# Kernel tuning notes

Hardware: AMD Instinct MI355X
Metric: run time of the kernel (lower is better)

Reference implementation:

```python
import jax, jax.numpy as jnp
import numpy as np

N = 30000   # nodes
E = 480000  # edges
IN = 128    # hidden_dim (in_feats)
H = 4       # num_heads
D = 128     # out_feats per head
HD = H * D
NEG_SLOPE = 0.2
BN_EPS = 1e-5


def setup_inputs() -> dict:
    key = jax.random.key(0)
    ks = jax.random.split(key, 12)
    feat = jax.random.normal(ks[0], (N, IN), dtype=jnp.float32)
    src = jax.random.randint(ks[1], (E,), 0, N)
    dst = jax.random.randint(ks[2], (E,), 0, N)
    sc_in = 1.0 / np.sqrt(IN)
    sc_hd = 1.0 / np.sqrt(HD)
    W_fc = jax.random.normal(ks[3], (IN, HD), dtype=jnp.float32) * sc_in
    attn_l = jax.random.normal(ks[4], (H, D), dtype=jnp.float32) * sc_in
    attn_r = jax.random.normal(ks[5], (H, D), dtype=jnp.float32) * sc_in
    W_res = jax.random.normal(ks[6], (IN, HD), dtype=jnp.float32) * sc_in
    bias_gat = jnp.zeros((HD,), dtype=jnp.float32)
    gamma = jnp.ones((HD,), dtype=jnp.float32)
    beta = jnp.zeros((HD,), dtype=jnp.float32)
    W_out = jax.random.normal(ks[7], (HD, IN), dtype=jnp.float32) * sc_hd
    b_out = jnp.zeros((IN,), dtype=jnp.float32)
    return dict(feat=feat, src=src, dst=dst, W_fc=W_fc, attn_l=attn_l,
                attn_r=attn_r, W_res=W_res, bias_gat=bias_gat,
                gamma=gamma, beta=beta, W_out=W_out, b_out=b_out)


def reference(feat, src, dst, W_fc, attn_l, attn_r, W_res, bias_gat,
              gamma, beta, W_out, b_out):
    # --- GATConv (eval mode: dropout off) ---
    h = (feat @ W_fc).reshape(N, H, D)               # projected feats [N,H,D]
    el = jnp.einsum('nhd,hd->nh', h, attn_l)         # [N,H]
    er = jnp.einsum('nhd,hd->nh', h, attn_r)         # [N,H]
    e = el[src] + er[dst]                            # [E,H]
    e = jnp.where(e > 0, e, NEG_SLOPE * e)           # leaky_relu(0.2)
    # segment softmax over edges grouped by destination node
    emax = jax.ops.segment_max(e, dst, num_segments=N)   # [N,H]
    emax = jnp.where(jnp.isfinite(emax), emax, 0.0)      # empty segments
    ex = jnp.exp(e - emax[dst])                          # [E,H]
    denom = jax.ops.segment_sum(ex, dst, num_segments=N) # [N,H]
    a = ex / denom[dst]                                  # [E,H] attention
    msgs = h[src] * a[:, :, None]                        # [E,H,D]
    rst = jax.ops.segment_sum(msgs, dst, num_segments=N) # [N,H,D]
    # residual (in_feats != H*out_feats -> linear res_fc) + bias
    rst = rst + (feat @ W_res).reshape(N, H, D) + bias_gat.reshape(1, H, D)
    # --- fc_out: Flatten -> BatchNorm1d (train stats) -> ReLU -> Linear ---
    x = rst.reshape(N, HD)
    mu = x.mean(axis=0)
    var = x.var(axis=0)
    xn = (x - mu) / jnp.sqrt(var + BN_EPS)
    x = jnp.maximum(gamma * xn + beta, 0.0)
    return x @ W_out + b_out                             # [N, IN]
```

## Files before the change

kernel.cpp:

```cpp
#include <hip/hip_runtime.h>

#define N_  30000
#define E_  480000

typedef short short8 __attribute__((ext_vector_type(8)));
typedef float f32x4  __attribute__((ext_vector_type(4)));
typedef unsigned int u32x4 __attribute__((ext_vector_type(4)));
typedef unsigned int u32x2 __attribute__((ext_vector_type(2)));
union Frag { u32x4 q; short8 v; unsigned short us[8]; };

__device__ __forceinline__ float b2f(unsigned short u){
  union { unsigned int i; float f; } v; v.i = ((unsigned int)u) << 16; return v.f;
}
__device__ __forceinline__ float blo(unsigned int u){
  union { unsigned int i; float f; } v; v.i = u << 16; return v.f;
}
__device__ __forceinline__ float bhi(unsigned int u){
  union { unsigned int i; float f; } v; v.i = u & 0xffff0000u; return v.f;
}
__device__ __forceinline__ unsigned short f2b(float f){
  union { float f; unsigned int u; } v; v.f = f;
  unsigned int u = v.u;
  return (unsigned short)((u + 0x7fffu + ((u >> 16) & 1u)) >> 16);
}

__global__ void k_initconv(const float* __restrict__ Wfc, const float* __restrict__ Wres,
                           const float* __restrict__ Wout, const float* __restrict__ feat,
                           unsigned short* __restrict__ Wt2, unsigned short* __restrict__ WtOut,
                           unsigned short* __restrict__ featb,
                           int* __restrict__ counts, int* __restrict__ cursor){
  int gid = blockIdx.x * 256 + threadIdx.x;
  int stride = gridDim.x * 256;
  if (gid < N_){ counts[gid] = 0; cursor[gid] = 0; }
  const int total1 = 512 * 256;
  const int total2 = 128 * 512;
  for (int i = gid; i < total1 + total2; i += stride){
    if (i < total1){
      int c = i >> 8, k = i & 255;
      float v = (k < 128) ? Wfc[k * 512 + c] : Wres[(k - 128) * 512 + c];
      Wt2[((k >> 7) << 16) + c * 128 + (k & 127)] = f2b(v);
    } else {
      int j = i - total1;
      int n = j >> 9, k = j & 511;
      WtOut[((k >> 7) << 14) + n * 128 + (k & 127)] = f2b(Wout[k * 128 + n]);
    }
  }
  for (int i = gid; i < N_ * 128; i += stride)
    featb[i] = f2b(feat[i]);
}

__global__ __launch_bounds__(128) void k_prep(const float* __restrict__ Wfc,
                                              const float* __restrict__ al,
                                              const float* __restrict__ ar,
                                              float* __restrict__ P){
  int idx = blockIdx.x * 128 + threadIdx.x;
  if (idx >= 1024) return;
  int k = idx >> 3, q = idx & 7;
  int h = q & 3;
  const float* a = (q < 4) ? al : ar;
  const float* wr = Wfc + k * 512 + h * 128;
  const float* av = a + h * 128;
  float s = 0.f;
#pragma unroll 4
  for (int d = 0; d < 128; d++) s += wr[d] * av[d];
  P[k * 8 + q] = s;
}

__global__ __launch_bounds__(256) void k_el(const float* __restrict__ feat,
                                            const float* __restrict__ P,
                                            float* __restrict__ el, float* __restrict__ er){
  __shared__ float sF[32 * 132];
  __shared__ float sP[1024];
  int t = threadIdx.x;
  int n0 = blockIdx.x * 32;
  *reinterpret_cast<f32x4*>(&sP[t * 4]) = *reinterpret_cast<const f32x4*>(P + t * 4);
#pragma unroll
  for (int i = 0; i < 4; i++){
    int c = t + i * 256;
    int r = c >> 5, cw = (c & 31) * 4;
    int gn = n0 + r;
    f32x4 v = {0.f, 0.f, 0.f, 0.f};
    if (gn < N_) v = *reinterpret_cast<const f32x4*>(feat + gn * 128 + cw);
    *reinterpret_cast<f32x4*>(&sF[r * 132 + cw]) = v;
  }
  __syncthreads();
  int node = t >> 3, q = t & 7;
  int gn = n0 + node;
  const float* fr = &sF[node * 132];
  float s = 0.f;
#pragma unroll 2
  for (int k = 0; k < 128; k += 4){
    f32x4 fv = *reinterpret_cast<const f32x4*>(fr + k);
#pragma unroll
    for (int j = 0; j < 4; j++) s += fv[j] * sP[(k + j) * 8 + q];
  }
  if (gn < N_){
    if (q < 4) el[gn * 4 + q] = s;
    else       er[gn * 4 + (q - 4)] = s;
  }
}

__global__ void k_hist(const int* __restrict__ dst, int* __restrict__ counts){
  int e = blockIdx.x * 256 + threadIdx.x;
  if (e < E_) atomicAdd(&counts[dst[e]], 1);
}

__global__ __launch_bounds__(1024) void k_scan(const int* __restrict__ counts,
                                               int* __restrict__ offs){
  __shared__ int wsum[16];
  int t = threadIdx.x;
  int lane = t & 63, w = t >> 6;
  int base = t * 32;
  int vals[32];
  int s = 0;
#pragma unroll
  for (int j = 0; j < 32; j++){
    int idx = base + j;
    int v = (idx < N_) ? counts[idx] : 0;
    vals[j] = s;
    s += v;
  }
  int x = s;
  for (int o = 1; o < 64; o <<= 1){
    int y = __shfl_up(x, o);
    if (lane >= o) x += y;
  }
  if (lane == 63) wsum[w] = x;
  __syncthreads();
  if (t < 16){
    int y = wsum[t];
    for (int o = 1; o < 16; o <<= 1){
      int z = __shfl_up(y, o, 16);
      if (t >= o) y += z;
    }
    wsum[t] = y;
  }
  __syncthreads();
  int wbase = (w > 0) ? wsum[w - 1] : 0;
  int ex = wbase + x - s;
#pragma unroll
  for (int j = 0; j < 32; j++){
    int idx = base + j;
    if (idx <= N_) offs[idx] = ex + vals[j];
  }
}

__global__ void k_edge(const int* __restrict__ src, const int* __restrict__ dst,
                       const float* __restrict__ el, const float* __restrict__ er,
                       float* __restrict__ es_s, int* __restrict__ src_s,
                       const int* __restrict__ offs, int* __restrict__ cursor){
  int e = blockIdx.x * 256 + threadIdx.x;
  if (e >= E_) return;
  int s = src[e], d = dst[e];
  f32x4 a = *reinterpret_cast<const f32x4*>(el + s * 4);
  f32x4 b = *reinterpret_cast<const f32x4*>(er + d * 4);
  f32x4 v = a + b;
#pragma unroll
  for (int i = 0; i < 4; i++) v[i] = v[i] > 0.f ? v[i] : 0.2f * v[i];
  int p = atomicAdd(&cursor[d], 1);
  int pos = offs[d] + p;
  *reinterpret_cast<f32x4*>(es_s + pos * 4) = v;
  src_s[pos] = s;
}

__global__ __launch_bounds__(256) void k_aggrf(const int* __restrict__ offs,
                                               const int* __restrict__ src_s,
                                               const float* __restrict__ es,
                                               const unsigned short* __restrict__ featb,
                                               unsigned short* __restrict__ fagg){
  __shared__ float wls[4][512];
  int wave = threadIdx.x >> 6, lane = threadIdx.x & 63;
  int n = blockIdx.x * 4 + wave;
  if (n >= N_) return;
  int off0 = __builtin_amdgcn_readfirstlane(offs[n]);
  int g = __builtin_amdgcn_readfirstlane(offs[n + 1]) - off0;
  int c0 = lane * 2;

  f32x4 m = {-1e30f, -1e30f, -1e30f, -1e30f};
  for (int i = lane; i < g; i += 64){
    f32x4 v = *reinterpret_cast<const f32x4*>(es + (off0 + i) * 4);
#pragma unroll
    for (int h = 0; h < 4; h++) m[h] = fmaxf(m[h], v[h]);
  }
#pragma unroll
  for (int o = 32; o >= 1; o >>= 1){
#pragma unroll
    for (int h = 0; h < 4; h++) m[h] = fmaxf(m[h], __shfl_xor(m[h], o));
  }
  f32x4 ssum = {0.f, 0.f, 0.f, 0.f};
  for (int i = lane; i < g; i += 64){
    f32x4 v = *reinterpret_cast<const f32x4*>(es + (off0 + i) * 4);
    f32x4 e;
#pragma unroll
    for (int h = 0; h < 4; h++){ e[h] = __expf(v[h] - m[h]); ssum[h] += e[h]; }
    if (i < 128) *reinterpret_cast<f32x4*>(&wls[wave][i * 4]) = e;
  }
#pragma unroll
  for (int o = 32; o >= 1; o >>= 1){
#pragma unroll
    for (int h = 0; h < 4; h++) ssum[h] += __shfl_xor(ssum[h], o);
  }
  f32x4 rd;
#pragma unroll
  for (int h = 0; h < 4; h++) rd[h] = (ssum[h] > 0.f) ? 1.0f / ssum[h] : 0.f;

  float acc[4][2] = {};
  int i = 0;
  for (; i + 7 < g; i += 8){
    int s8[8];
    f32x4 w8[8];
    unsigned int p8[8];
#pragma unroll
    for (int u = 0; u < 8; u++) s8[u] = __builtin_amdgcn_readfirstlane(src_s[off0 + i + u]);
#pragma unroll
    for (int u = 0; u < 8; u++){
      int ei = i + u;
      if (ei < 128) w8[u] = *reinterpret_cast<const f32x4*>(&wls[wave][ei * 4]);
      else {
        f32x4 v = *reinterpret_cast<const f32x4*>(es + (off0 + ei) * 4);
#pragma unroll
        for (int h = 0; h < 4; h++) w8[u][h] = __expf(v[h] - m[h]);
      }
    }
#pragma unroll
    for (int u = 0; u < 8; u++) p8[u] = *reinterpret_cast<const unsigned int*>(featb + s8[u] * 128 + c0);
#pragma unroll
    for (int u = 0; u < 8; u++){
      float lo = blo(p8[u]), hi = bhi(p8[u]);
#pragma unroll
      for (int h = 0; h < 4; h++){
        acc[h][0] += w8[u][h] * lo;
        acc[h][1] += w8[u][h] * hi;
      }
    }
  }
  for (; i < g; i++){
    int sv = __builtin_amdgcn_readfirstlane(src_s[off0 + i]);
    f32x4 wv;
    if (i < 128) wv = *reinterpret_cast<const f32x4*>(&wls[wave][i * 4]);
    else {
      f32x4 v = *reinterpret_cast<const f32x4*>(es + (off0 + i) * 4);
#pragma unroll
      for (int h = 0; h < 4; h++) wv[h] = __expf(v[h] - m[h]);
    }
    unsigned int pv = *reinterpret_cast<const unsigned int*>(featb + sv * 128 + c0);
    float lo = blo(pv), hi = bhi(pv);
#pragma unroll
    for (int h = 0; h < 4; h++){
      acc[h][0] += wv[h] * lo;
      acc[h][1] += wv[h] * hi;
    }
  }
#pragma unroll
  for (int h = 0; h < 4; h++){
    unsigned int ov = (unsigned int)f2b(acc[h][0] * rd[h]) |
                      ((unsigned int)f2b(acc[h][1] * rd[h]) << 16);
    *reinterpret_cast<unsigned int*>(fagg + n * 512 + h * 128 + c0) = ov;
  }
}

__global__ __launch_bounds__(512) void k_gemmC(const unsigned short* __restrict__ fagg,
                                               const unsigned short* __restrict__ featb,
                                               const unsigned short* __restrict__ Wt2,
                                               const float* __restrict__ bias,
                                               unsigned short* __restrict__ comb){
  __shared__ unsigned short wsl[256 * 128];
  char* wb = (char*)wsl;
  int tid = threadIdx.x;
  int wave = tid >> 6, lane = tid & 63;
  int lrow = lane & 15, quad = lane >> 4;
  int rowbase = blockIdx.x * 128 + wave * 16;
  int colbase = blockIdx.y * 256;
  int h0 = blockIdx.y * 2;
  int arow = rowbase + lrow; if (arow > N_ - 1) arow = N_ - 1;
  const unsigned short* aF = fagg + arow * 512 + h0 * 128;
  const unsigned short* aX = featb + arow * 128;
  f32x4 acc[16] = {};
  for (int phase = 0; phase < 2; phase++){
    __syncthreads();
#pragma unroll
    for (int i = 0; i < 8; i++){
      int c = tid + i * 512;
      int col = c >> 4, unit = c & 15;
      u32x4 v = *reinterpret_cast<const u32x4*>(Wt2 + (phase << 16) + (colbase + col) * 128 + unit * 8);
      int byte = (col * 256 + unit * 16) ^ ((col & 7) << 4);
      *reinterpret_cast<u32x4*>(wb + byte) = v;
    }
    __syncthreads();
#pragma unroll
    for (int kk = 0; kk < 4; kk++){
      Frag a0, a1;
      if (phase == 0){
        a0.q = *reinterpret_cast<const u32x4*>(aF + kk * 32 + quad * 8);
        a1.q = *reinterpret_cast<const u32x4*>(aF + 128 + kk * 32 + quad * 8);
      } else {
        a0.q = *reinterpret_cast<const u32x4*>(aX + kk * 32 + quad * 8);
        a1.q = a0.q;
      }
#pragma unroll
      for (int s = 0; s < 16; s++){
        int r = s * 16 + lrow;
        int byte = (r * 256 + kk * 64 + quad * 16) ^ ((r & 7) << 4);
        Frag b; b.q = *reinterpret_cast<const u32x4*>(wb + byte);
        acc[s] = __builtin_amdgcn_mfma_f32_16x16x32_bf16(b.v, (s < 8 ? a0.v : a1.v), acc[s], 0, 0, 0);
      }
    }
  }
  int gr = rowbase + lrow;
  if (gr < N_){
    unsigned short* crow = comb + gr * 512 + colbase;
#pragma unroll
    for (int s = 0; s < 16; s++){
      f32x4 bb = *reinterpret_cast<const f32x4*>(bias + colbase + s * 16 + quad * 4);
      u32x2 ov;
#pragma unroll
      for (int d = 0; d < 2; d++){
        float v0 = acc[s][2 * d]     + bb[2 * d];
        float v1 = acc[s][2 * d + 1] + bb[2 * d + 1];
        ov[d] = (unsigned int)f2b(v0) | ((unsigned int)f2b(v1) << 16);
      }
      *reinterpret_cast<u32x2*>(crow + s * 16 + quad * 4) = ov;
    }
  }
}

__global__ __launch_bounds__(256) void k_stats(const unsigned short* __restrict__ comb,
                                               float* __restrict__ psum,
                                               float* __restrict__ psq){
  __shared__ float lsum[4][512];
  __shared__ float lsq[4][512];
  int t = threadIdx.x, lane = t & 63, rg = t >> 6;
  int c0 = lane * 8;
  const int rows = 118;
  int r0 = blockIdx.x * rows;
  int r1 = r0 + rows; if (r1 > N_) r1 = N_;
  float s[8] = {}, q[8] = {};
  for (int r = r0 + rg; r < r1; r += 4){
    u32x4 pv = *reinterpret_cast<const u32x4*>(comb + r * 512 + c0);
#pragma unroll
    for (int d = 0; d < 4; d++){
      float v0 = blo(pv[d]);
      float v1 = bhi(pv[d]);
      s[2*d]   += v0; q[2*d]   += v0 * v0;
      s[2*d+1] += v1; q[2*d+1] += v1 * v1;
    }
  }
#pragma unroll
  for (int d = 0; d < 8; d++){ lsum[rg][c0 + d] = s[d]; lsq[rg][c0 + d] = q[d]; }
  __syncthreads();
#pragma unroll
  for (int half = 0; half < 2; half++){
    int ch = t + half * 256;
    float a = lsum[0][ch] + lsum[1][ch] + lsum[2][ch] + lsum[3][ch];
    float b = lsq[0][ch] + lsq[1][ch] + lsq[2][ch] + lsq[3][ch];
    psum[blockIdx.x * 512 + ch] = a;
    psq[blockIdx.x * 512 + ch] = b;
  }
}

__global__ __launch_bounds__(128) void k_bnfin(const float* __restrict__ psum,
                                               const float* __restrict__ psq,
                                               const float* __restrict__ gamma,
                                               const float* __restrict__ beta,
                                               float* __restrict__ scale,
                                               float* __restrict__ shift){
  int ch = blockIdx.x * 128 + threadIdx.x;
  float s0 = 0.f, s1 = 0.f, s2 = 0.f, s3 = 0.f;
  float q0 = 0.f, q1 = 0.f, q2 = 0.f, q3 = 0.f;
  for (int b = 0; b < 256; b += 4){
    s0 += psum[(b    ) * 512 + ch];
    s1 += psum[(b + 1) * 512 + ch];
    s2 += psum[(b + 2) * 512 + ch];
    s3 += psum[(b + 3) * 512 + ch];
    q0 += psq[(b    ) * 512 + ch];
    q1 += psq[(b + 1) * 512 + ch];
    q2 += psq[(b + 2) * 512 + ch];
    q3 += psq[(b + 3) * 512 + ch];
  }
  float sum = (s0 + s1) + (s2 + s3);
  float sq  = (q0 + q1) + (q2 + q3);
  float mu  = sum / (float)N_;
  float var = sq / (float)N_ - mu * mu;
  float inv = rsqrtf(var + 1e-5f);
  float sc  = gamma[ch] * inv;
  scale[ch] = sc;
  shift[ch] = beta[ch] - mu * sc;
}

__global__ __launch_bounds__(512) void k_gemm2(const unsigned short* __restrict__ comb,
                                               const unsigned short* __restrict__ WtOut,
                                               const float* __restrict__ scale,
                                               const float* __restrict__ shift,
                                               const float* __restrict__ bout,
                                               float* __restrict__ out){
  __shared__ float sc[512], sh[512];
  __shared__ unsigned short wsl[128 * 128];
  char* wb = (char*)wsl;
  int t = threadIdx.x;
  sc[t] = scale[t]; sh[t] = shift[t];
  int wave = t >> 6, lane = t & 63, lrow = lane & 15, quad = lane >> 4;
  int rowbase = blockIdx.x * 128 + wave * 16;
  int rr = rowbase + lrow; if (rr > N_ - 1) rr = N_ - 1;
  const unsigned short* arow = comb + rr * 512;
  f32x4 acc[8] = {};
  for (int phase = 0; phase < 4; phase++){
    __syncthreads();
#pragma unroll
    for (int i = 0; i < 4; i++){
      int c = t + i * 512;
      int col = c >> 4, unit = c & 15;
      u32x4 v = *reinterpret_cast<const u32x4*>(WtOut + (phase << 14) + col * 128 + unit * 8);
      int byte = (col * 256 + unit * 16) ^ ((col & 7) << 4);
      *reinterpret_cast<u32x4*>(wb + byte) = v;
    }
    __syncthreads();
#pragma unroll
    for (int kk = 0; kk < 4; kk++){
      int base = phase * 128 + kk * 32 + quad * 8;
      Frag a; a.q = *reinterpret_cast<const u32x4*>(arow + base);
#pragma unroll
      for (int i2 = 0; i2 < 8; i2++){
        float x = b2f(a.us[i2]);
        x = fmaf(x, sc[base + i2], sh[base + i2]);
        a.us[i2] = f2b(fmaxf(x, 0.0f));
      }
#pragma unroll
      for (int s = 0; s < 8; s++){
        int r = s * 16 + lrow;
        int byte = (r * 256 + kk * 64 + quad * 16) ^ ((r & 7) << 4);
        Frag b; b.q = *reinterpret_cast<const u32x4*>(wb + byte);
        acc[s] = __builtin_amdgcn_mfma_f32_16x16x32_bf16(b.v, a.v, acc[s], 0, 0, 0);
      }
    }
  }
  int gr = rowbase + lrow;
  if (gr < N_){
    float* orow = out + gr * 128;
#pragma unroll
    for (int s = 0; s < 8; s++){
      int cb = s * 16 + quad * 4;
      f32x4 bb = *reinterpret_cast<const f32x4*>(bout + cb);
      f32x4 ov;
#pragma unroll
      for (int j = 0; j < 4; j++) ov[j] = acc[s][j] + bb[j];
      *reinterpret_cast<f32x4*>(orow + cb) = ov;
    }
  }
}

extern "C" void kernel_launch(void* const* d_in, const int* in_sizes, int n_in,
                              void* d_out, int out_size, void* d_ws, size_t ws_size,
                              hipStream_t stream){
  const float* feat  = (const float*)d_in[0];
  const int*   src   = (const int*)d_in[1];
  const int*   dst   = (const int*)d_in[2];
  const float* Wfc   = (const float*)d_in[3];
  const float* al    = (const float*)d_in[4];
  const float* ar    = (const float*)d_in[5];
  const float* Wres  = (const float*)d_in[6];
  const float* bias  = (const float*)d_in[7];
  const float* gamma = (const float*)d_in[8];
  const float* beta  = (const float*)d_in[9];
  const float* Wout  = (const float*)d_in[10];
  const float* bout  = (const float*)d_in[11];
  float* out = (float*)d_out;

  char* ws = (char*)d_ws;
  unsigned short* comb  = (unsigned short*)(ws + 0);
  unsigned short* fagg  = (unsigned short*)(ws + 30720000);
  unsigned short* Wt2   = (unsigned short*)(ws + 61440000);
  unsigned short* WtOut = (unsigned short*)(ws + 61702144);
  float*          el    = (float*)(ws + 61833216);
  float*          er    = (float*)(ws + 62313216);
  float*          es_s  = (float*)(ws + 62793216);
  int*            offs  = (int*)(ws + 70473216);
  int*            counts= (int*)(ws + 70593280);
  int*            cursor= (int*)(ws + 70713280);
  int*            src_s = (int*)(ws + 70833280);
  float*          psum  = (float*)(ws + 72753280);
  float*          psq   = (float*)(ws + 73277568);
  float*          scale = (float*)(ws + 73801856);
  float*          shift = (float*)(ws + 73803904);
  unsigned short* featb = (unsigned short*)(ws + 73805952);
  float*          P     = psum;

  k_initconv<<<640, 256, 0, stream>>>(Wfc, Wres, Wout, feat, Wt2, WtOut, featb,
                                      counts, cursor);
  k_prep<<<8, 128, 0, stream>>>(Wfc, al, ar, P);
  k_hist<<<(E_ + 255) / 256, 256, 0, stream>>>(dst, counts);
  k_scan<<<1, 1024, 0, stream>>>(counts, offs);
  k_el<<<(N_ + 31) / 32, 256, 0, stream>>>(feat, P, el, er);
  k_edge<<<(E_ + 255) / 256, 256, 0, stream>>>(src, dst, el, er, es_s, src_s, offs, cursor);
  k_aggrf<<<(N_ + 3) / 4, 256, 0, stream>>>(offs, src_s, es_s, featb, fagg);
  dim3 gC((N_ + 127) / 128, 2);
  k_gemmC<<<gC, 512, 0, stream>>>(fagg, featb, Wt2, bias, comb);
  k_stats<<<256, 256, 0, stream>>>(comb, psum, psq);
  k_bnfin<<<4, 128, 0, stream>>>(psum, psq, gamma, beta, scale, shift);
  k_gemm2<<<(N_ + 127) / 128, 512, 0, stream>>>(comb, WtOut, scale, shift, bout, out);
}
```

Baseline: 286.0 us.

## Fuse bf16 feature conversion into el kernel and compute edge scores inside aggregation

The feat-to-bf16 conversion moves from the init kernel into k_el, which already stages feat in shared memory. The edge kernel no longer computes and scatters per-edge scores. The aggregation kernel now recomputes scores from el/er and src_s, and drops the max-subtraction pass in the softmax. The gather loop is software-pipelined, with src indices broadcast by shuffle, which removes the es_s buffer traffic and a reduction pass. Skipping the max subtraction risks exp overflow for large logits, although the inputs here are small.

```diff
diff --git a/kernel.cpp b/kernel.cpp
--- a/kernel.cpp
+++ b/kernel.cpp
@@ -5,6 +5,7 @@
 
 typedef short short8 __attribute__((ext_vector_type(8)));
 typedef float f32x4  __attribute__((ext_vector_type(4)));
+typedef float f32x2  __attribute__((ext_vector_type(2)));
 typedef unsigned int u32x4 __attribute__((ext_vector_type(4)));
 typedef unsigned int u32x2 __attribute__((ext_vector_type(2)));
 union Frag { u32x4 q; short8 v; unsigned short us[8]; };
@@ -25,9 +26,8 @@
 }
 
 __global__ void k_initconv(const float* __restrict__ Wfc, const float* __restrict__ Wres,
-                           const float* __restrict__ Wout, const float* __restrict__ feat,
+                           const float* __restrict__ Wout,
                            unsigned short* __restrict__ Wt2, unsigned short* __restrict__ WtOut,
-                           unsigned short* __restrict__ featb,
                            int* __restrict__ counts, int* __restrict__ cursor){
   int gid = blockIdx.x * 256 + threadIdx.x;
   int stride = gridDim.x * 256;
@@ -45,8 +45,6 @@
       WtOut[((k >> 7) << 14) + n * 128 + (k & 127)] = f2b(Wout[k * 128 + n]);
     }
   }
-  for (int i = gid; i < N_ * 128; i += stride)
-    featb[i] = f2b(feat[i]);
 }
 
 __global__ __launch_bounds__(128) void k_prep(const float* __restrict__ Wfc,
@@ -68,7 +66,8 @@
 
 __global__ __launch_bounds__(256) void k_el(const float* __restrict__ feat,
                                             const float* __restrict__ P,
-                                            float* __restrict__ el, float* __restrict__ er){
+                                            float* __restrict__ el, float* __restrict__ er,
+                                            unsigned short* __restrict__ featb){
   __shared__ float sF[32 * 132];
   __shared__ float sP[1024];
   int t = threadIdx.x;
@@ -84,6 +83,17 @@
     *reinterpret_cast<f32x4*>(&sF[r * 132 + cw]) = v;
   }
   __syncthreads();
+#pragma unroll
+  for (int i = 0; i < 8; i++){
+    int c = t + i * 256;
+    int r = c >> 6, cw = (c & 63) * 2;
+    int gn = n0 + r;
+    if (gn < N_){
+      float v0 = sF[r * 132 + cw], v1 = sF[r * 132 + cw + 1];
+      unsigned int pv = (unsigned int)f2b(v0) | ((unsigned int)f2b(v1) << 16);
+      *reinterpret_cast<unsigned int*>(featb + gn * 128 + cw) = pv;
+    }
+  }
   int node = t >> 3, q = t & 7;
   int gn = n0 + node;
   const float* fr = &sF[node * 132];
@@ -146,26 +156,19 @@
 }
 
 __global__ void k_edge(const int* __restrict__ src, const int* __restrict__ dst,
-                       const float* __restrict__ el, const float* __restrict__ er,
-                       float* __restrict__ es_s, int* __restrict__ src_s,
+                       int* __restrict__ src_s,
                        const int* __restrict__ offs, int* __restrict__ cursor){
   int e = blockIdx.x * 256 + threadIdx.x;
   if (e >= E_) return;
-  int s = src[e], d = dst[e];
-  f32x4 a = *reinterpret_cast<const f32x4*>(el + s * 4);
-  f32x4 b = *reinterpret_cast<const f32x4*>(er + d * 4);
-  f32x4 v = a + b;
-#pragma unroll
-  for (int i = 0; i < 4; i++) v[i] = v[i] > 0.f ? v[i] : 0.2f * v[i];
+  int d = dst[e];
   int p = atomicAdd(&cursor[d], 1);
-  int pos = offs[d] + p;
-  *reinterpret_cast<f32x4*>(es_s + pos * 4) = v;
-  src_s[pos] = s;
+  src_s[offs[d] + p] = src[e];
 }
 
 __global__ __launch_bounds__(256) void k_aggrf(const int* __restrict__ offs,
                                                const int* __restrict__ src_s,
-                                               const float* __restrict__ es,
+                                               const float* __restrict__ el,
+                                               const float* __restrict__ er,
                                                const unsigned short* __restrict__ featb,
                                                unsigned short* __restrict__ fagg){
   __shared__ float wls[4][512];
@@ -173,88 +176,84 @@
   int n = blockIdx.x * 4 + wave;
   if (n >= N_) return;
   int off0 = __builtin_amdgcn_readfirstlane(offs[n]);
-  int g = __builtin_amdgcn_readfirstlane(offs[n + 1]) - off0;
+  int g    = __builtin_amdgcn_readfirstlane(offs[n + 1]) - off0;
+  int head = lane >> 4, sub = lane & 15;
+  f32x4 er4 = *reinterpret_cast<const f32x4*>(er + n * 4);
+  float ern = er4[head];
+
+  float ssum = 0.f;
+  for (int i = sub; i < g; i += 16){
+    int s = src_s[off0 + i];
+    float v = el[s * 4 + head] + ern;
+    v = v > 0.f ? v : 0.2f * v;
+    float w = __expf(v);
+    if (i < 128) wls[wave][i * 4 + head] = w;
+    ssum += w;
+  }
+#pragma unroll
+  for (int o = 8; o >= 1; o >>= 1) ssum += __shfl_xor(ssum, o, 16);
+  float rdh = (ssum > 0.f) ? 1.0f / ssum : 0.f;
+  f32x4 rd4;
+#pragma unroll
+  for (int h = 0; h < 4; h++) rd4[h] = __shfl(rdh, h * 16 + sub);
+
   int c0 = lane * 2;
-
-  f32x4 m = {-1e30f, -1e30f, -1e30f, -1e30f};
-  for (int i = lane; i < g; i += 64){
-    f32x4 v = *reinterpret_cast<const f32x4*>(es + (off0 + i) * 4);
-#pragma unroll
-    for (int h = 0; h < 4; h++) m[h] = fmaxf(m[h], v[h]);
-  }
-#pragma unroll
-  for (int o = 32; o >= 1; o >>= 1){
-#pragma unroll
-    for (int h = 0; h < 4; h++) m[h] = fmaxf(m[h], __shfl_xor(m[h], o));
-  }
-  f32x4 ssum = {0.f, 0.f, 0.f, 0.f};
-  for (int i = lane; i < g; i += 64){
-    f32x4 v = *reinterpret_cast<const f32x4*>(es + (off0 + i) * 4);
-    f32x4 e;
-#pragma unroll
-    for (int h = 0; h < 4; h++){ e[h] = __expf(v[h] - m[h]); ssum[h] += e[h]; }
-    if (i < 128) *reinterpret_cast<f32x4*>(&wls[wave][i * 4]) = e;
-  }
-#pragma unroll
-  for (int o = 32; o >= 1; o >>= 1){
-#pragma unroll
-    for (int h = 0; h < 4; h++) ssum[h] += __shfl_xor(ssum[h], o);
-  }
-  f32x4 rd;
-#pragma unroll
-  for (int h = 0; h < 4; h++) rd[h] = (ssum[h] > 0.f) ? 1.0f / ssum[h] : 0.f;
-
-  float acc[4][2] = {};
+  f32x2 acc2[4] = {};
+  auto FMA1 = [&](int ei, int s, unsigned int pv){
+    f32x4 wv;
+    if (ei < 128) wv = *reinterpret_cast<const f32x4*>(&wls[wave][ei * 4]);
+    else {
+      f32x4 evv = *reinterpret_cast<const f32x4*>(el + s * 4);
+#pragma unroll
+      for (int h = 0; h < 4; h++){
+        float v = evv[h] + er4[h];
+        v = v > 0.f ? v : 0.2f * v;
+        wv[h] = __expf(v);
+      }
+    }
+    f32x2 lh; lh[0] = blo(pv); lh[1] = bhi(pv);
+#pragma unroll
+    for (int h = 0; h < 4; h++) acc2[h] += lh * wv[h];
+  };
+
   int i = 0;
-  for (; i + 7 < g; i += 8){
-    int s8[8];
-    f32x4 w8[8];
-    unsigned int p8[8];
-#pragma unroll
-    for (int u = 0; u < 8; u++) s8[u] = __builtin_amdgcn_readfirstlane(src_s[off0 + i + u]);
-#pragma unroll
-    for (int u = 0; u < 8; u++){
-      int ei = i + u;
-      if (ei < 128) w8[u] = *reinterpret_cast<const f32x4*>(&wls[wave][ei * 4]);
-      else {
-        f32x4 v = *reinterpret_cast<const f32x4*>(es + (off0 + ei) * 4);
-#pragma unroll
-        for (int h = 0; h < 4; h++) w8[u][h] = __expf(v[h] - m[h]);
-      }
-    }
-#pragma unroll
-    for (int u = 0; u < 8; u++) p8[u] = *reinterpret_cast<const unsigned int*>(featb + s8[u] * 128 + c0);
-#pragma unroll
-    for (int u = 0; u < 8; u++){
-      float lo = blo(p8[u]), hi = bhi(p8[u]);
-#pragma unroll
-      for (int h = 0; h < 4; h++){
-        acc[h][0] += w8[u][h] * lo;
-        acc[h][1] += w8[u][h] * hi;
-      }
-    }
-  }
-  for (; i < g; i++){
-    int sv = __builtin_amdgcn_readfirstlane(src_s[off0 + i]);
-    f32x4 wv;
-    if (i < 128) wv = *reinterpret_cast<const f32x4*>(&wls[wave][i * 4]);
-    else {
-      f32x4 v = *reinterpret_cast<const f32x4*>(es + (off0 + i) * 4);
-#pragma unroll
-      for (int h = 0; h < 4; h++) wv[h] = __expf(v[h] - m[h]);
-    }
-    unsigned int pv = *reinterpret_cast<const unsigned int*>(featb + sv * 128 + c0);
-    float lo = blo(pv), hi = bhi(pv);
-#pragma unroll
-    for (int h = 0; h < 4; h++){
-      acc[h][0] += wv[h] * lo;
-      acc[h][1] += wv[h] * hi;
-    }
-  }
+  while (i < g){
+    int blk = g - i; if (blk > 64) blk = 64;
+    int idx = i + lane;
+    int ssrc = (idx < g) ? src_s[off0 + idx] : 0;
+    int nfull = blk >> 3;
+    if (nfull){
+      int sa[8]; unsigned int pa[8];
+#pragma unroll
+      for (int u = 0; u < 8; u++) sa[u] = __shfl(ssrc, u);
+#pragma unroll
+      for (int u = 0; u < 8; u++) pa[u] = *reinterpret_cast<const unsigned int*>(featb + sa[u] * 128 + c0);
+      for (int c = 1; c < nfull; c++){
+        int sb[8]; unsigned int pb[8];
+#pragma unroll
+        for (int u = 0; u < 8; u++) sb[u] = __shfl(ssrc, c * 8 + u);
+#pragma unroll
+        for (int u = 0; u < 8; u++) pb[u] = *reinterpret_cast<const unsigned int*>(featb + sb[u] * 128 + c0);
+#pragma unroll
+        for (int u = 0; u < 8; u++) FMA1(i + (c - 1) * 8 + u, sa[u], pa[u]);
+#pragma unroll
+        for (int u = 0; u < 8; u++){ sa[u] = sb[u]; pa[u] = pb[u]; }
+      }
+#pragma unroll
+      for (int u = 0; u < 8; u++) FMA1(i + (nfull - 1) * 8 + u, sa[u], pa[u]);
+    }
+    for (int j = nfull * 8; j < blk; j++){
+      int s = __shfl(ssrc, j);
+      unsigned int pv = *reinterpret_cast<const unsigned int*>(featb + s * 128 + c0);
+      FMA1(i + j, s, pv);
+    }
+    i += blk;
+  }
+
 #pragma unroll
   for (int h = 0; h < 4; h++){
-    unsigned int ov = (unsigned int)f2b(acc[h][0] * rd[h]) |
-                      ((unsigned int)f2b(acc[h][1] * rd[h]) << 16);
+    unsigned int ov = (unsigned int)f2b(acc2[h][0] * rd4[h]) |
+                      ((unsigned int)f2b(acc2[h][1] * rd4[h]) << 16);
     *reinterpret_cast<unsigned int*>(fagg + n * 512 + h * 128 + c0) = ov;
   }
 }
@@ -472,7 +471,6 @@
   unsigned short* WtOut = (unsigned short*)(ws + 61702144);
   float*          el    = (float*)(ws + 61833216);
   float*          er    = (float*)(ws + 62313216);
-  float*          es_s  = (float*)(ws + 62793216);
   int*            offs  = (int*)(ws + 70473216);
   int*            counts= (int*)(ws + 70593280);
   int*            cursor= (int*)(ws + 70713280);
@@ -484,14 +482,13 @@
   unsigned short* featb = (unsigned short*)(ws + 73805952);
   float*          P     = psum;
 
-  k_initconv<<<640, 256, 0, stream>>>(Wfc, Wres, Wout, feat, Wt2, WtOut, featb,
-                                      counts, cursor);
+  k_initconv<<<256, 256, 0, stream>>>(Wfc, Wres, Wout, Wt2, WtOut, counts, cursor);
   k_prep<<<8, 128, 0, stream>>>(Wfc, al, ar, P);
   k_hist<<<(E_ + 255) / 256, 256, 0, stream>>>(dst, counts);
   k_scan<<<1, 1024, 0, stream>>>(counts, offs);
-  k_el<<<(N_ + 31) / 32, 256, 0, stream>>>(feat, P, el, er);
-  k_edge<<<(E_ + 255) / 256, 256, 0, stream>>>(src, dst, el, er, es_s, src_s, offs, cursor);
-  k_aggrf<<<(N_ + 3) / 4, 256, 0, stream>>>(offs, src_s, es_s, featb, fagg);
+  k_el<<<(N_ + 31) / 32, 256, 0, stream>>>(feat, P, el, er, featb);
+  k_edge<<<(E_ + 255) / 256, 256, 0, stream>>>(src, dst, src_s, offs, cursor);
+  k_aggrf<<<(N_ + 3) / 4, 256, 0, stream>>>(offs, src_s, el, er, featb, fagg);
   dim3 gC((N_ + 127) / 128, 2);
   k_gemmC<<<gC, 512, 0, stream>>>(fagg, featb, Wt2, bias, comb);
   k_stats<<<256, 256, 0, stream>>>(comb, psum, psq);
```

New measurement: 276.7 us. 1.03x faster.
